# Performance work log

Measured on AMD Instinct MI355X. Metric: run time of the kernel, lower is better.

Reference implementation:

```python
import jax, jax.numpy as jnp
import numpy as np
from jax import lax

D_MODEL = 1024
STATE_DIM = 32
GROUPS = 8
GROUP_DIM = D_MODEL // GROUPS
DT_MIN = 0.001
DT_MAX = 0.1
EPS = 1e-6


def setup_inputs() -> dict:
    key = jax.random.key(0)
    ks = jax.random.split(key, 6)
    B, T = 4, 4096
    u = jax.random.normal(ks[0], (B, T, D_MODEL), dtype=jnp.float32)
    state = jnp.zeros((B, GROUPS, STATE_DIM), dtype=jnp.float32)
    A_log = jax.random.normal(ks[1], (GROUPS, STATE_DIM), dtype=jnp.float32) * 0.02
    B_param = jax.random.normal(ks[2], (GROUPS, STATE_DIM, GROUP_DIM), dtype=jnp.float32) * 0.02
    C = jax.random.normal(ks[3], (GROUPS, GROUP_DIM, STATE_DIM), dtype=jnp.float32) * 0.02
    Dp = jnp.zeros((GROUPS, GROUP_DIM), dtype=jnp.float32)
    dt_logit = jnp.zeros((GROUPS,), dtype=jnp.float32)
    return {"u": u, "state": state, "A_log": A_log, "B_param": B_param,
            "C": C, "Dp": Dp, "dt_logit": dt_logit}


def reference(u, state, A_log, B_param, C, Dp, dt_logit):
    Bsz, T, Dm = u.shape
    A = -jax.nn.softplus(A_log)                                  # [G,N]
    dt = DT_MIN + (DT_MAX - DT_MIN) * jax.nn.sigmoid(dt_logit)   # [G]
    dt_g = dt[:, None]                                           # [G,1]
    Abar = jnp.exp(A * dt_g)                                     # [G,N]
    # (exp(A dt) - 1)/A, stable for small |A|
    frac = jnp.where(jnp.abs(A) > EPS, (Abar - 1.0) / A,
                     jnp.broadcast_to(dt_g, A.shape))            # [G,N]
    Bbar = frac[..., None] * B_param                             # [G,N,gd]

    u_g = u.reshape(Bsz, T, GROUPS, GROUP_DIM)                   # [B,T,G,gd]
    # precompute input injections for all timesteps, then scan the LTI recurrence
    Bu = jnp.einsum('btgi,gni->btgn', u_g, Bbar)                 # [B,T,G,N]
    Bu_t = jnp.moveaxis(Bu, 1, 0)                                # [T,B,G,N]

    def step(s, bu):
        s = s * Abar + bu                                        # [B,G,N]
        return s, s

    s_final, states = lax.scan(step, state, Bu_t)                # states: [T,B,G,N]
    Cs = jnp.einsum('tbgn,gdn->btgd', states, C)                 # [B,T,G,gd]
    y = (Cs + Dp * u_g).reshape(Bsz, T, Dm)                      # [B,T,D]
    return y, s_final
```

## Files before the change

kernel.cpp:

```cpp
#include <hip/hip_runtime.h>
#include <hip/hip_bf16.h>

#define DM 1024
#define SD 32
#define NG 8
#define GD 128
#define BS 4
#define TT 4096
#define CL 64
#define NC (TT/CL)

typedef __attribute__((ext_vector_type(8))) short short8;
typedef __attribute__((ext_vector_type(4))) float f32x4;

#define WS_POWA  0
#define WS_STL   65536
#define WS_CARRY (WS_STL + 8388608)
#define WS_PAL   (WS_CARRY + 262144)

__device__ __forceinline__ unsigned short f2bf(float f) {
  __hip_bfloat16 h = __float2bfloat16(f);
  return __builtin_bit_cast(unsigned short, h);
}
__device__ __forceinline__ float bf2f(unsigned short h) {
  return __uint_as_float(((unsigned)h) << 16);
}
__device__ __forceinline__ float softplus_f(float x) {
  return (x > 20.f) ? x : log1pf(expf(x));
}
__device__ __forceinline__ short8 pack8(float4 a, float4 b) {
  short8 h;
  h[0]=(short)f2bf(a.x); h[1]=(short)f2bf(a.y); h[2]=(short)f2bf(a.z); h[3]=(short)f2bf(a.w);
  h[4]=(short)f2bf(b.x); h[5]=(short)f2bf(b.y); h[6]=(short)f2bf(b.z); h[7]=(short)f2bf(b.w);
  return h;
}

__global__ __launch_bounds__(64, 2) void ka_bu_scan(const float* __restrict__ u,
                                                    const float* __restrict__ A_log,
                                                    const float* __restrict__ B_param,
                                                    const float* __restrict__ dt_logit,
                                                    unsigned char* __restrict__ ws) {
  const int bx = blockIdx.x;
  const int c = bx & (NC - 1);
  const int g = (bx >> 6) & (NG - 1);
  const int b = bx >> 9;
  const int l = threadIdx.x;
  const int lr = l & 15, lh = l >> 4;
  const int n = l & 31;
  const int seg = l >> 5;

  const float* up = u + ((size_t)b * TT + (size_t)c * CL) * DM + g * GD;
  float4 ub[4][4][2];
  #pragma unroll
  for (int kt = 0; kt < 4; ++kt)
    #pragma unroll
    for (int m = 0; m < 4; ++m) {
      const float* p = up + (size_t)(m * 16 + lr) * DM + kt * 32 + lh * 8;
      ub[kt][m][0] = *(const float4*)p;
      ub[kt][m][1] = *(const float4*)(p + 4);
    }

  const float dtg = 0.001f + 0.099f * (1.f / (1.f + expf(-dt_logit[g])));

  float fracv[2];
  #pragma unroll
  for (int nt = 0; nt < 2; ++nt) {
    int np = nt * 16 + lr;
    float A = -softplus_f(A_log[g * SD + np]);
    float a = expf(A * dtg);
    fracv[nt] = (fabsf(A) > 1e-6f) ? (a - 1.f) / A : dtg;
  }
  float a_n;
  {
    float A = -softplus_f(A_log[g * SD + n]);
    a_n = expf(A * dtg);
  }

  const float* bp = B_param + (size_t)g * SD * GD;
  short8 bfr[4][2];
  #pragma unroll
  for (int kt = 0; kt < 4; ++kt)
    #pragma unroll
    for (int nt = 0; nt < 2; ++nt) {
      const float* p = bp + (size_t)(nt * 16 + lr) * GD + kt * 32 + lh * 8;
      float4 v0 = *(const float4*)p;
      float4 v1 = *(const float4*)(p + 4);
      float s = fracv[nt];
      v0.x*=s; v0.y*=s; v0.z*=s; v0.w*=s;
      v1.x*=s; v1.y*=s; v1.z*=s; v1.w*=s;
      bfr[kt][nt] = pack8(v0, v1);
    }

  f32x4 acc[4][2];
  #pragma unroll
  for (int m = 0; m < 4; ++m)
    #pragma unroll
    for (int nt = 0; nt < 2; ++nt)
      #pragma unroll
      for (int j = 0; j < 4; ++j) acc[m][nt][j] = 0.f;

  #pragma unroll
  for (int kt = 0; kt < 4; ++kt) {
    short8 af[4];
    #pragma unroll
    for (int m = 0; m < 4; ++m)
      af[m] = pack8(ub[kt][m][0], ub[kt][m][1]);
    #pragma unroll
    for (int m = 0; m < 4; ++m)
      #pragma unroll
      for (int nt = 0; nt < 2; ++nt)
        acc[m][nt] = __builtin_amdgcn_mfma_f32_16x16x32_bf16(af[m], bfr[kt][nt], acc[m][nt], 0, 0, 0);
  }

  __shared__ __align__(16) float sBu[CL * 33];
  __shared__ __align__(16) unsigned short sSt[CL * SD];
  #pragma unroll
  for (int m = 0; m < 4; ++m)
    #pragma unroll
    for (int nt = 0; nt < 2; ++nt)
      #pragma unroll
      for (int j = 0; j < 4; ++j) {
        int t = m * 16 + lh * 4 + j;
        sBu[t * 33 + (nt * 16 + lr)] = acc[m][nt][j];
      }
  __syncthreads();

  float sloc[32];
  float s = 0.f;
  #pragma unroll
  for (int t = 0; t < 32; ++t) {
    s = fmaf(s, a_n, sBu[(seg * 32 + t) * 33 + n]);
    sloc[t] = s;
  }
  const float s31 = __shfl(s, n);
  float* carry = (float*)(ws + WS_CARRY);
  {
    float pw = 1.f;
    float vlast = 0.f;
    #pragma unroll
    for (int t = 0; t < 32; ++t) {
      pw *= a_n;
      float v = seg ? fmaf(pw, s31, sloc[t]) : sloc[t];
      sSt[(seg * 32 + t) * SD + n] = f2bf(v);
      vlast = v;
    }
    if (seg)
      carry[((b * NG + g) * NC + c) * SD + n] = vlast;
  }
  __syncthreads();

  unsigned short* stg = (unsigned short*)(ws + WS_STL) + ((size_t)((b * NC + c) * NG + g)) * CL * SD;
  #pragma unroll
  for (int p = 0; p < 4; ++p) {
    int off = (p * 64 + l) * 8;
    *(short8*)(stg + off) = *(short8*)(sSt + off);
  }

  if (b == 0 && c == 0 && l < SD) {
    float* powA = (float*)(ws + WS_POWA);
    float* powAL = (float*)(ws + WS_PAL);
    float p = 1.f;
    #pragma unroll
    for (int t = 0; t < CL; ++t) {
      p *= a_n;
      powA[(g * CL + t) * SD + l] = p;
    }
    float aL = p;
    float q = 1.f;
    #pragma unroll
    for (int j = 0; j < CL; ++j) {
      powAL[(g * CL + j) * SD + l] = q;
      q *= aL;
    }
  }
}

__global__ __launch_bounds__(128) void kb_y(const float* __restrict__ u,
                                            const float* __restrict__ state0,
                                            const float* __restrict__ C,
                                            const float* __restrict__ Dp,
                                            unsigned char* __restrict__ ws,
                                            float* __restrict__ y,
                                            float* __restrict__ sfin) {
  const int bx = blockIdx.x;
  const int c = bx & (NC - 1);
  const int g = (bx >> 6) & (NG - 1);
  const int b = bx >> 9;
  const int tid = threadIdx.x;
  const int w = tid >> 6;
  const int l = tid & 63;
  const int lr = l & 15, lh = l >> 4;
  const int n = l & 31;

  const float* powA = (const float*)(ws + WS_POWA) + g * CL * SD;
  const float* powAL = (const float*)(ws + WS_PAL) + g * CL * SD;
  const float* carry = (const float*)(ws + WS_CARRY) + (size_t)(b * NG + g) * NC * SD;
  const unsigned short* stg = (const unsigned short*)(ws + WS_STL) + ((size_t)((b * NC + c) * NG + g)) * CL * SD;

  __shared__ __align__(16) float sY[32 * 132];

  bool need_u;
  {
    float2 dpc = *(const float2*)(Dp + g * GD + l * 2);
    need_u = __ballot((dpc.x != 0.f) || (dpc.y != 0.f)) != 0ULL;
  }

  float p;
  {
    float a0 = 0.f, a1 = 0.f, a2 = 0.f, a3 = 0.f;
    int cc = 0;
    while (cc + 8 <= c) {
      float ca[8], wt[8];
      #pragma unroll
      for (int e = 0; e < 8; ++e) {
        ca[e] = carry[(cc + e) * SD + n];
        wt[e] = powAL[(c - 1 - cc - e) * SD + n];
      }
      a0 = fmaf(wt[0], ca[0], a0); a1 = fmaf(wt[1], ca[1], a1);
      a2 = fmaf(wt[2], ca[2], a2); a3 = fmaf(wt[3], ca[3], a3);
      a0 = fmaf(wt[4], ca[4], a0); a1 = fmaf(wt[5], ca[5], a1);
      a2 = fmaf(wt[6], ca[6], a2); a3 = fmaf(wt[7], ca[7], a3);
      cc += 8;
    }
    for (; cc < c; ++cc)
      a0 = fmaf(powAL[(c - 1 - cc) * SD + n], carry[cc * SD + n], a0);
    p = fmaf(state0[(b * NG + g) * SD + n], powAL[c * SD + n], (a0 + a1) + (a2 + a3));
  }
  if (w == 0 && c == NC - 1 && l < SD) {
    const float aL = powA[(CL - 1) * SD + l];
    sfin[(b * NG + g) * SD + l] = fmaf(p, aL, carry[(NC - 1) * SD + l]);
  }

  float pr[8];
  #pragma unroll
  for (int e = 0; e < 8; ++e) pr[e] = __shfl(p, lh * 8 + e);

  short8 sf[4];
  #pragma unroll
  for (int tt = 0; tt < 4; ++tt) {
    int t = tt * 16 + lr;
    short8 sl = *(const short8*)(stg + t * SD + lh * 8);
    const float* pw = powA + t * SD + lh * 8;
    float4 pw0 = *(const float4*)pw;
    float4 pw1 = *(const float4*)(pw + 4);
    short8 hh;
    hh[0] = (short)f2bf(bf2f((unsigned short)sl[0]) + pw0.x * pr[0]);
    hh[1] = (short)f2bf(bf2f((unsigned short)sl[1]) + pw0.y * pr[1]);
    hh[2] = (short)f2bf(bf2f((unsigned short)sl[2]) + pw0.z * pr[2]);
    hh[3] = (short)f2bf(bf2f((unsigned short)sl[3]) + pw0.w * pr[3]);
    hh[4] = (short)f2bf(bf2f((unsigned short)sl[4]) + pw1.x * pr[4]);
    hh[5] = (short)f2bf(bf2f((unsigned short)sl[5]) + pw1.y * pr[5]);
    hh[6] = (short)f2bf(bf2f((unsigned short)sl[6]) + pw1.z * pr[6]);
    hh[7] = (short)f2bf(bf2f((unsigned short)sl[7]) + pw1.w * pr[7]);
    sf[tt] = hh;
  }

  const float* cp = C + (size_t)g * GD * SD;
  const size_t rowbase = ((size_t)b * TT + (size_t)c * CL) * DM + g * GD;

  short8 cf[4];
  #pragma unroll
  for (int dd = 0; dd < 4; ++dd) {
    int d = (w * 4 + dd) * 16 + lr;
    const float* pp = cp + (size_t)d * SD + lh * 8;
    float4 v0 = *(const float4*)pp;
    float4 v1 = *(const float4*)(pp + 4);
    cf[dd] = pack8(v0, v1);
  }
  f32x4 acc[4][4];
  #pragma unroll
  for (int dd = 0; dd < 4; ++dd)
    #pragma unroll
    for (int tt = 0; tt < 4; ++tt) {
      f32x4 z;
      #pragma unroll
      for (int j = 0; j < 4; ++j) z[j] = 0.f;
      acc[dd][tt] = __builtin_amdgcn_mfma_f32_16x16x32_bf16(cf[dd], sf[tt], z, 0, 0, 0);
    }

  const int sd4 = (tid & 31) * 4;
  float4 dpv = *(const float4*)(Dp + g * GD + sd4);

  #pragma unroll
  for (int tp = 0; tp < 2; ++tp) {
    if (tp) __syncthreads();
    #pragma unroll
    for (int dd = 0; dd < 4; ++dd)
      #pragma unroll
      for (int q = 0; q < 2; ++q) {
        int tt = tp * 2 + q;
        int tl = q * 16 + lr;
        int d0 = (w * 4 + dd) * 16 + lh * 4;
        *(float4*)(sY + tl * 132 + d0) = (float4){acc[dd][tt][0], acc[dd][tt][1],
                                                  acc[dd][tt][2], acc[dd][tt][3]};
      }
    __syncthreads();
    #pragma unroll
    for (int r = 0; r < 8; ++r) {
      int tl = r * 4 + (tid >> 5);
      int t = tp * 32 + tl;
      float4 v = *(const float4*)(sY + tl * 132 + sd4);
      size_t off = rowbase + (size_t)t * DM + sd4;
      if (need_u) {
        float4 u4 = *(const float4*)(u + off);
        v.x += dpv.x * u4.x; v.y += dpv.y * u4.y;
        v.z += dpv.z * u4.z; v.w += dpv.w * u4.w;
      }
      *(float4*)(y + off) = v;
    }
  }
}

extern "C" void kernel_launch(void* const* d_in, const int* in_sizes, int n_in,
                              void* d_out, int out_size, void* d_ws, size_t ws_size,
                              hipStream_t stream) {
  const float* u       = (const float*)d_in[0];
  const float* state0  = (const float*)d_in[1];
  const float* A_log   = (const float*)d_in[2];
  const float* B_param = (const float*)d_in[3];
  const float* C       = (const float*)d_in[4];
  const float* Dp      = (const float*)d_in[5];
  const float* dtl     = (const float*)d_in[6];
  float* y = (float*)d_out;
  unsigned char* ws = (unsigned char*)d_ws;
  float* sfin = y + (size_t)BS * TT * DM;

  ka_bu_scan<<<dim3(BS * NG * NC), dim3(64), 0, stream>>>(u, A_log, B_param, dtl, ws);
  kb_y<<<dim3(BS * NG * NC), dim3(128), 0, stream>>>(u, state0, C, Dp, ws, y, sfin);
}
```

Before: 43.86 us.

## Widen both kernels to four waves and stage scaled B in swizzled LDS

The Bu-and-scan kernel moves from one wave to four waves per block. Each wave loads 16 time rows of u and software-prefetches the second half of its K slices while the first MFMAs run. The discretized B is built once per block into XOR-swizzled shared memory instead of being loaded in full by every lane. The y kernel also goes to 256 threads, each wave handling two d-tiles instead of four. The aim is more memory-level parallelism and less register pressure for the bandwidth-bound u/y traffic, at the cost of extra barriers and a sequential scan that now runs on only one of four waves.

```diff
diff --git a/kernel.cpp b/kernel.cpp
--- a/kernel.cpp
+++ b/kernel.cpp
@@ -35,106 +35,105 @@
   return h;
 }
 
-__global__ __launch_bounds__(64, 2) void ka_bu_scan(const float* __restrict__ u,
-                                                    const float* __restrict__ A_log,
-                                                    const float* __restrict__ B_param,
-                                                    const float* __restrict__ dt_logit,
-                                                    unsigned char* __restrict__ ws) {
+__global__ __launch_bounds__(256) void ka_bu_scan(const float* __restrict__ u,
+                                                  const float* __restrict__ A_log,
+                                                  const float* __restrict__ B_param,
+                                                  const float* __restrict__ dt_logit,
+                                                  unsigned char* __restrict__ ws) {
   const int bx = blockIdx.x;
   const int c = bx & (NC - 1);
   const int g = (bx >> 6) & (NG - 1);
   const int b = bx >> 9;
-  const int l = threadIdx.x;
+  const int tid = threadIdx.x;
+  const int w = tid >> 6;
+  const int l = tid & 63;
   const int lr = l & 15, lh = l >> 4;
   const int n = l & 31;
   const int seg = l >> 5;
 
-  const float* up = u + ((size_t)b * TT + (size_t)c * CL) * DM + g * GD;
-  float4 ub[4][4][2];
-  #pragma unroll
-  for (int kt = 0; kt < 4; ++kt)
-    #pragma unroll
-    for (int m = 0; m < 4; ++m) {
-      const float* p = up + (size_t)(m * 16 + lr) * DM + kt * 32 + lh * 8;
-      ub[kt][m][0] = *(const float4*)p;
-      ub[kt][m][1] = *(const float4*)(p + 4);
-    }
+  __shared__ __align__(16) unsigned char sMem[12544];
 
   const float dtg = 0.001f + 0.099f * (1.f / (1.f + expf(-dt_logit[g])));
 
-  float fracv[2];
-  #pragma unroll
-  for (int nt = 0; nt < 2; ++nt) {
-    int np = nt * 16 + lr;
-    float A = -softplus_f(A_log[g * SD + np]);
+  const float* urow = u + ((size_t)b * TT + (size_t)c * CL + w * 16 + lr) * DM + g * GD;
+  float4 ub[2][2];
+  #pragma unroll
+  for (int kt = 0; kt < 2; ++kt) {
+    ub[kt][0] = *(const float4*)(urow + kt * 32 + lh * 8);
+    ub[kt][1] = *(const float4*)(urow + kt * 32 + lh * 8 + 4);
+  }
+
+  {
+    const int nB = tid >> 3;
+    const int i0 = (tid & 7) * 16;
+    float A = -softplus_f(A_log[g * SD + nB]);
     float a = expf(A * dtg);
-    fracv[nt] = (fabsf(A) > 1e-6f) ? (a - 1.f) / A : dtg;
-  }
+    float frac = (fabsf(A) > 1e-6f) ? (a - 1.f) / A : dtg;
+    const float* p = B_param + (size_t)g * SD * GD + (size_t)nB * GD + i0;
+    float4 v0 = *(const float4*)p;
+    float4 v1 = *(const float4*)(p + 4);
+    float4 v2 = *(const float4*)(p + 8);
+    float4 v3 = *(const float4*)(p + 12);
+    v0.x*=frac; v0.y*=frac; v0.z*=frac; v0.w*=frac;
+    v1.x*=frac; v1.y*=frac; v1.z*=frac; v1.w*=frac;
+    v2.x*=frac; v2.y*=frac; v2.z*=frac; v2.w*=frac;
+    v3.x*=frac; v3.y*=frac; v3.z*=frac; v3.w*=frac;
+    const int swz = (nB & 7) << 4;
+    const int base = nB * 256 + i0 * 2;
+    *(short8*)(sMem + ((base) ^ swz))      = pack8(v0, v1);
+    *(short8*)(sMem + ((base + 16) ^ swz)) = pack8(v2, v3);
+  }
+
   float a_n;
   {
     float A = -softplus_f(A_log[g * SD + n]);
     a_n = expf(A * dtg);
   }
-
-  const float* bp = B_param + (size_t)g * SD * GD;
-  short8 bfr[4][2];
-  #pragma unroll
-  for (int kt = 0; kt < 4; ++kt)
+  __syncthreads();
+
+  f32x4 acc[2];
+  #pragma unroll
+  for (int nt = 0; nt < 2; ++nt)
+    #pragma unroll
+    for (int j = 0; j < 4; ++j) acc[nt][j] = 0.f;
+
+  #pragma unroll
+  for (int kt = 0; kt < 4; ++kt) {
+    short8 af = pack8(ub[kt & 1][0], ub[kt & 1][1]);
+    if (kt < 2) {
+      ub[kt & 1][0] = *(const float4*)(urow + (kt + 2) * 32 + lh * 8);
+      ub[kt & 1][1] = *(const float4*)(urow + (kt + 2) * 32 + lh * 8 + 4);
+    }
     #pragma unroll
     for (int nt = 0; nt < 2; ++nt) {
-      const float* p = bp + (size_t)(nt * 16 + lr) * GD + kt * 32 + lh * 8;
-      float4 v0 = *(const float4*)p;
-      float4 v1 = *(const float4*)(p + 4);
-      float s = fracv[nt];
-      v0.x*=s; v0.y*=s; v0.z*=s; v0.w*=s;
-      v1.x*=s; v1.y*=s; v1.z*=s; v1.w*=s;
-      bfr[kt][nt] = pack8(v0, v1);
-    }
-
-  f32x4 acc[4][2];
-  #pragma unroll
-  for (int m = 0; m < 4; ++m)
-    #pragma unroll
-    for (int nt = 0; nt < 2; ++nt)
-      #pragma unroll
-      for (int j = 0; j < 4; ++j) acc[m][nt][j] = 0.f;
-
-  #pragma unroll
-  for (int kt = 0; kt < 4; ++kt) {
-    short8 af[4];
-    #pragma unroll
-    for (int m = 0; m < 4; ++m)
-      af[m] = pack8(ub[kt][m][0], ub[kt][m][1]);
-    #pragma unroll
-    for (int m = 0; m < 4; ++m)
-      #pragma unroll
-      for (int nt = 0; nt < 2; ++nt)
-        acc[m][nt] = __builtin_amdgcn_mfma_f32_16x16x32_bf16(af[m], bfr[kt][nt], acc[m][nt], 0, 0, 0);
-  }
-
-  __shared__ __align__(16) float sBu[CL * 33];
-  __shared__ __align__(16) unsigned short sSt[CL * SD];
-  #pragma unroll
-  for (int m = 0; m < 4; ++m)
-    #pragma unroll
-    for (int nt = 0; nt < 2; ++nt)
-      #pragma unroll
-      for (int j = 0; j < 4; ++j) {
-        int t = m * 16 + lh * 4 + j;
-        sBu[t * 33 + (nt * 16 + lr)] = acc[m][nt][j];
-      }
+      const int np = nt * 16 + lr;
+      short8 bf8 = *(const short8*)(sMem + ((np * 256 + kt * 64 + lh * 16) ^ ((np & 7) << 4)));
+      acc[nt] = __builtin_amdgcn_mfma_f32_16x16x32_bf16(af, bf8, acc[nt], 0, 0, 0);
+    }
+  }
   __syncthreads();
 
-  float sloc[32];
-  float s = 0.f;
-  #pragma unroll
-  for (int t = 0; t < 32; ++t) {
-    s = fmaf(s, a_n, sBu[(seg * 32 + t) * 33 + n]);
-    sloc[t] = s;
-  }
-  const float s31 = __shfl(s, n);
+  float* sBu = (float*)sMem;
+  unsigned short* sSt = (unsigned short*)(sMem + 8448);
+  #pragma unroll
+  for (int nt = 0; nt < 2; ++nt)
+    #pragma unroll
+    for (int j = 0; j < 4; ++j) {
+      int t = w * 16 + lh * 4 + j;
+      sBu[t * 33 + (nt * 16 + lr)] = acc[nt][j];
+    }
+  __syncthreads();
+
   float* carry = (float*)(ws + WS_CARRY);
-  {
+  if (w == 0) {
+    float sloc[32];
+    float s = 0.f;
+    #pragma unroll
+    for (int t = 0; t < 32; ++t) {
+      s = fmaf(s, a_n, sBu[(seg * 32 + t) * 33 + n]);
+      sloc[t] = s;
+    }
+    const float s31 = __shfl(s, n);
     float pw = 1.f;
     float vlast = 0.f;
     #pragma unroll
@@ -150,32 +149,28 @@
   __syncthreads();
 
   unsigned short* stg = (unsigned short*)(ws + WS_STL) + ((size_t)((b * NC + c) * NG + g)) * CL * SD;
-  #pragma unroll
-  for (int p = 0; p < 4; ++p) {
-    int off = (p * 64 + l) * 8;
-    *(short8*)(stg + off) = *(short8*)(sSt + off);
-  }
-
-  if (b == 0 && c == 0 && l < SD) {
+  *(short8*)(stg + tid * 8) = *(short8*)(sSt + tid * 8);
+
+  if (b == 0 && c == 0 && tid < SD) {
     float* powA = (float*)(ws + WS_POWA);
     float* powAL = (float*)(ws + WS_PAL);
     float p = 1.f;
     #pragma unroll
     for (int t = 0; t < CL; ++t) {
       p *= a_n;
-      powA[(g * CL + t) * SD + l] = p;
+      powA[(g * CL + t) * SD + tid] = p;
     }
     float aL = p;
     float q = 1.f;
     #pragma unroll
     for (int j = 0; j < CL; ++j) {
-      powAL[(g * CL + j) * SD + l] = q;
+      powAL[(g * CL + j) * SD + tid] = q;
       q *= aL;
     }
   }
 }
 
-__global__ __launch_bounds__(128) void kb_y(const float* __restrict__ u,
+__global__ __launch_bounds__(256) void kb_y(const float* __restrict__ u,
                                             const float* __restrict__ state0,
                                             const float* __restrict__ C,
                                             const float* __restrict__ Dp,
@@ -258,18 +253,18 @@
   const float* cp = C + (size_t)g * GD * SD;
   const size_t rowbase = ((size_t)b * TT + (size_t)c * CL) * DM + g * GD;
 
-  short8 cf[4];
-  #pragma unroll
-  for (int dd = 0; dd < 4; ++dd) {
-    int d = (w * 4 + dd) * 16 + lr;
+  short8 cf[2];
+  #pragma unroll
+  for (int dd = 0; dd < 2; ++dd) {
+    int d = (w * 2 + dd) * 16 + lr;
     const float* pp = cp + (size_t)d * SD + lh * 8;
     float4 v0 = *(const float4*)pp;
     float4 v1 = *(const float4*)(pp + 4);
     cf[dd] = pack8(v0, v1);
   }
-  f32x4 acc[4][4];
-  #pragma unroll
-  for (int dd = 0; dd < 4; ++dd)
+  f32x4 acc[2][4];
+  #pragma unroll
+  for (int dd = 0; dd < 2; ++dd)
     #pragma unroll
     for (int tt = 0; tt < 4; ++tt) {
       f32x4 z;
@@ -285,19 +280,19 @@
   for (int tp = 0; tp < 2; ++tp) {
     if (tp) __syncthreads();
     #pragma unroll
-    for (int dd = 0; dd < 4; ++dd)
+    for (int dd = 0; dd < 2; ++dd)
       #pragma unroll
       for (int q = 0; q < 2; ++q) {
         int tt = tp * 2 + q;
         int tl = q * 16 + lr;
-        int d0 = (w * 4 + dd) * 16 + lh * 4;
+        int d0 = (w * 2 + dd) * 16 + lh * 4;
         *(float4*)(sY + tl * 132 + d0) = (float4){acc[dd][tt][0], acc[dd][tt][1],
                                                   acc[dd][tt][2], acc[dd][tt][3]};
       }
     __syncthreads();
     #pragma unroll
-    for (int r = 0; r < 8; ++r) {
-      int tl = r * 4 + (tid >> 5);
+    for (int r = 0; r < 4; ++r) {
+      int tl = r * 8 + (tid >> 5);
       int t = tp * 32 + tl;
       float4 v = *(const float4*)(sY + tl * 132 + sd4);
       size_t off = rowbase + (size_t)t * DM + sd4;
@@ -325,6 +320,6 @@
   unsigned char* ws = (unsigned char*)d_ws;
   float* sfin = y + (size_t)BS * TT * DM;
 
-  ka_bu_scan<<<dim3(BS * NG * NC), dim3(64), 0, stream>>>(u, A_log, B_param, dtl, ws);
-  kb_y<<<dim3(BS * NG * NC), dim3(128), 0, stream>>>(u, state0, C, Dp, ws, y, sfin);
-}
+  ka_bu_scan<<<dim3(BS * NG * NC), dim3(256), 0, stream>>>(u, A_log, B_param, dtl, ws);
+  kb_y<<<dim3(BS * NG * NC), dim3(256), 0, stream>>>(u, state0, C, Dp, ws, y, sfin);
+}
```

Result: slower. 51.81 us (+18.1%).
